# Kernel optimization log

Hardware: AMD Instinct MI355X
Metric: run time of the kernel (lower is better)

## Reference

```python
import math
import jax, jax.numpy as jnp
import numpy as np

N = 100_000          # nodes
D = 128              # sample.num_node_features
E = 1_600_000        # edges (avg degree 16)
ACM = 4              # augmented_channels_multiplier
C = 128              # channels = 4*4*channels_optuna(=8)
RATIO = 0.7          # topk_ratio + 0.1
FINAL_NODES = 3


def setup_inputs() -> dict:
    key = jax.random.key(0)
    ks = jax.random.split(key, 14)
    s = 0.05
    x = jax.random.normal(ks[0], (N, D), jnp.float32)
    edge_index = jax.random.randint(ks[1], (2, E), 0, N, dtype=jnp.int32)
    # dense_input GraphConv(D, ACM): called with empty edges -> only lin_root weight + lin_rel bias matter
    Wd_root = jax.random.normal(ks[2], (ACM, D), jnp.float32) * s
    bd = jax.random.normal(ks[3], (ACM,), jnp.float32) * s
    # input GraphConv(ACM, C)
    Wi_rel = jax.random.normal(ks[4], (C, ACM), jnp.float32) * s
    bi = jax.random.normal(ks[5], (C,), jnp.float32) * s
    Wi_root = jax.random.normal(ks[6], (C, ACM), jnp.float32) * s
    # TopKPooling(C) attention vector
    p = jax.random.normal(ks[7], (C,), jnp.float32) * s
    # conv1 GraphConv(C, 2C)
    W1_rel = jax.random.normal(ks[8], (2 * C, C), jnp.float32) * s
    b1 = jax.random.normal(ks[9], (2 * C,), jnp.float32) * s
    W1_root = jax.random.normal(ks[10], (2 * C, C), jnp.float32) * s
    # output Linear(3 * 2C, 1)
    Wo = jax.random.normal(ks[11], (1, FINAL_NODES * 2 * C), jnp.float32) * s
    bo = jax.random.normal(ks[12], (1,), jnp.float32) * s
    return {"x": x, "edge_index": edge_index, "Wd_root": Wd_root, "bd": bd,
            "Wi_rel": Wi_rel, "bi": bi, "Wi_root": Wi_root, "p": p,
            "W1_rel": W1_rel, "b1": b1, "W1_root": W1_root, "Wo": Wo, "bo": bo}


def reference(x, edge_index, Wd_root, bd, Wi_rel, bi, Wi_root, p, W1_rel, b1, W1_root, Wo, bo):
    n = x.shape[0]
    src, dst = edge_index[0], edge_index[1]  # messages flow src -> dst

    # dense_input GraphConv with empty edge set: aggr == 0 -> lin_rel bias + lin_root(x)
    h = jax.nn.gelu(x @ Wd_root.T + bd, approximate=False)               # [N, ACM]

    # input GraphConv(ACM, C): out = lin_rel(sum_j x_j) + lin_root(x)
    aggr = jax.ops.segment_sum(h[src], dst, num_segments=n)              # [N, ACM]
    h = jax.nn.gelu(aggr @ Wi_rel.T + bi + h @ Wi_root.T, approximate=False)  # [N, C]

    # TopKPooling(C, ratio=0.7): score = tanh(x.p / ||p||), keep top-k, scale kept x by score
    k = int(math.ceil(RATIO * n))
    score = jnp.tanh((h @ p) / jnp.linalg.norm(p))                        # [N]
    top_scores, perm = jax.lax.top_k(score, k)
    hp = h[perm] * top_scores[:, None]                                    # [k, C]
    # remap edges: kept node -> new index, dropped -> sentinel k
    inv = jnp.full((n,), k, dtype=jnp.int32).at[perm].set(jnp.arange(k, dtype=jnp.int32))
    ns, nd = inv[src], inv[dst]
    valid = (ns < k) & (nd < k)

    # conv1 GraphConv(C, 2C) on coarsened graph (masked scatter, sentinel row dropped)
    msg = jnp.where(valid[:, None], hp[jnp.minimum(ns, k - 1)], 0.0)      # [E, C]
    aggr = jax.ops.segment_sum(msg, jnp.where(valid, nd, k), num_segments=k + 1)[:k]
    h2 = jax.nn.gelu(aggr @ W1_rel.T + b1 + hp @ W1_root.T, approximate=False)  # [k, 2C]

    # avg_pool_x with cluster = i % 3 over single-graph batch
    cluster = jnp.arange(k, dtype=jnp.int32) % FINAL_NODES
    sums = jax.ops.segment_sum(h2, cluster, num_segments=FINAL_NODES)
    counts = jax.ops.segment_sum(jnp.ones((k,), h2.dtype), cluster, num_segments=FINAL_NODES)
    pooled = sums / counts[:, None]                                       # [3, 2C]

    # output Linear on flattened vector -> shape [1]
    return pooled.reshape(-1) @ Wo.T + bo
```

## Files before the change

### kernel.cpp

```cpp
#include <hip/hip_runtime.h>
#include <stdint.h>

#define N_NODES 100000
#define D_FEAT  128
#define E_EDGES 1600000
#define ACMC    4
#define CCH     128
#define C2CH    256
#define KKEEP   70000
#define KPAD    70016
#define NBLK    547
#define BINCAP  64
#define NBINS   (1 << 20)
#define NWIN    8
#define WWIN    12500

#define NB_BUILD (1563 * NWIN)
#define NB_H1    (N_NODES / 4)
#define NB_WCONV 128
#define NB_FRONT (NB_BUILD + NB_H1 + NB_WCONV)

typedef unsigned int u32;
typedef unsigned long long u64;
typedef unsigned short u16;
typedef short bf16x8 __attribute__((ext_vector_type(8)));
typedef float f32x4 __attribute__((ext_vector_type(4)));
typedef int i32x4 __attribute__((ext_vector_type(4)));

__device__ __forceinline__ float gelu_exact(float v){
    return 0.5f * v * (1.0f + erff(v * 0.70710678118654752440f));
}
__device__ __forceinline__ float bflo(u32 v){ return __uint_as_float(v << 16); }
__device__ __forceinline__ float bfhi(u32 v){ return __uint_as_float(v & 0xFFFF0000u); }
__device__ __forceinline__ u16 f2bf(float f){
    u32 x = __float_as_uint(f);
    return (u16)((x + 0x7FFFu + ((x >> 16) & 1u)) >> 16);
}

__global__ __launch_bounds__(256) void k_front(const int* __restrict__ ei,
                                               int* __restrict__ deg,
                                               int* __restrict__ slot,
                                               const float* __restrict__ x,
                                               const float* __restrict__ Wd,
                                               const float* __restrict__ bd,
                                               float* __restrict__ h1,
                                               const float* __restrict__ Wrel,
                                               const float* __restrict__ Wroot,
                                               u16* __restrict__ wcat) {
    int b = blockIdx.x;
    if (b < NB_BUILD) {
        int win = b & (NWIN - 1);
        int chunk = b >> 3;
        int e0 = (chunk * 256 + threadIdx.x) * 4;
        if (e0 >= E_EDGES) return;
        i32x4 dv = __builtin_nontemporal_load((const i32x4*)(ei + E_EDGES + e0));
        i32x4 sv = __builtin_nontemporal_load((const i32x4*)(ei + e0));
        int lo = win * WWIN, hi = lo + WWIN;
        #pragma unroll
        for (int j = 0; j < 4; j++) {
            int d = dv[j];
            if (d >= lo && d < hi) {
                int pos = atomicAdd(&deg[d], 1);
                if (pos < BINCAP) slot[d * BINCAP + pos] = sv[j];
            }
        }
        return;
    }
    if (b < NB_BUILD + NB_H1) {
        int tid = threadIdx.x;
        int wid = tid >> 6, lane = tid & 63;
        int node = (b - NB_BUILD) * 4 + wid;
        const float2* xr = (const float2*)(x + (size_t)node * D_FEAT);
        float2 v = xr[lane];
        const float2* wd = (const float2*)Wd;
        float s[4];
        #pragma unroll
        for (int j = 0; j < 4; j++) {
            float2 w = wd[j * 64 + lane];
            s[j] = v.x * w.x + v.y * w.y;
        }
        #pragma unroll
        for (int off = 32; off > 0; off >>= 1) {
            #pragma unroll
            for (int j = 0; j < 4; j++) s[j] += __shfl_xor(s[j], off);
        }
        if (lane == 0) {
            float4 o;
            o.x = gelu_exact(s[0] + bd[0]);
            o.y = gelu_exact(s[1] + bd[1]);
            o.z = gelu_exact(s[2] + bd[2]);
            o.w = gelu_exact(s[3] + bd[3]);
            ((float4*)h1)[node] = o;
        }
        return;
    }
    {
        int g = (b - NB_BUILD - NB_H1) * 256 + threadIdx.x;
        int ch = g >> 7, t = g & 127;
        wcat[(size_t)ch * 256 + t]       = f2bf(Wrel[(size_t)ch * 128 + t]);
        wcat[(size_t)ch * 256 + 128 + t] = f2bf(Wroot[(size_t)ch * 128 + t]);
    }
}

__global__ __launch_bounds__(256) void k_aggr1g(const int* __restrict__ deg,
                                                const int* __restrict__ slot,
                                                const float* __restrict__ h1,
                                                float* __restrict__ aggr1) {
    int d = blockIdx.x * blockDim.x + threadIdx.x;
    if (d >= N_NODES) return;
    int cnt = deg[d]; if (cnt > BINCAP) cnt = BINCAP;
    int base = d * BINCAP;
    float4 acc = make_float4(0.f, 0.f, 0.f, 0.f);
    for (int i0 = 0; i0 < cnt; i0 += 8) {
        int m = cnt - i0; if (m > 8) m = 8;
        int ss[8];
        #pragma unroll
        for (int j = 0; j < 8; j++) {
            int sj = slot[base + i0 + j];
            ss[j] = (j < m) ? sj : 0;
        }
        float4 vv[8];
        #pragma unroll
        for (int j = 0; j < 8; j++) vv[j] = ((const float4*)h1)[ss[j]];
        #pragma unroll
        for (int j = 0; j < 8; j++) {
            float msk = (j < m) ? 1.f : 0.f;
            acc.x += msk * vv[j].x;
            acc.y += msk * vv[j].y;
            acc.z += msk * vv[j].z;
            acc.w += msk * vv[j].w;
        }
    }
    ((float4*)aggr1)[d] = acc;
}

__global__ __launch_bounds__(256) void k_h_score(const float* __restrict__ aggr1,
                                                 const float* __restrict__ h1,
                                                 const float* __restrict__ Wi_rel,
                                                 const float* __restrict__ bi,
                                                 const float* __restrict__ Wi_root,
                                                 const float* __restrict__ p,
                                                 u16* __restrict__ hsb,
                                                 u32* __restrict__ dkey,
                                                 int* __restrict__ hist) {
    __shared__ float4 swr[128], swo[128];
    __shared__ float sbi[128], spv[128];
    __shared__ float spred[2];
    __shared__ float red[2][2];
    __shared__ float sscore[2];
    int tid = threadIdx.x;
    if (tid < 128) {
        swr[tid] = ((const float4*)Wi_rel)[tid];
        swo[tid] = ((const float4*)Wi_root)[tid];
        sbi[tid] = bi[tid];
        spv[tid] = p[tid];
    }
    __syncthreads();
    if (tid < 128) {
        float pp = spv[tid] * spv[tid];
        #pragma unroll
        for (int off = 32; off > 0; off >>= 1) pp += __shfl_xor(pp, off);
        if ((tid & 63) == 0) spred[tid >> 6] = pp;
    }
    __syncthreads();
    float pnorm = sqrtf(spred[0] + spred[1]);

    int half = tid >> 7;
    int c = tid & 127;
    int wih = (tid >> 6) & 1;
    int lane = tid & 63;
    float4 wr = swr[c], wo = swo[c];
    float bic = sbi[c], pc = spv[c];

    for (int node = blockIdx.x * 2 + half; node < N_NODES; node += gridDim.x * 2) {
        float4 ag = ((const float4*)aggr1)[node];
        float4 hv = ((const float4*)h1)[node];
        float val = ag.x * wr.x + ag.y * wr.y + ag.z * wr.z + ag.w * wr.w
                  + hv.x * wo.x + hv.y * wo.y + hv.z * wo.z + hv.w * wo.w
                  + bic;
        float g = gelu_exact(val);
        float hp = g * pc;
        #pragma unroll
        for (int off = 32; off > 0; off >>= 1) hp += __shfl_xor(hp, off);
        if (lane == 0) red[half][wih] = hp;
        __syncthreads();
        if (c == 0) {
            float H = red[half][0] + red[half][1];
            float sc = tanhf(H / pnorm);
            sscore[half] = sc;
            u32 u = __float_as_uint(sc);
            u32 asc = (u & 0x80000000u) ? ~u : (u | 0x80000000u);
            u32 d = ~asc;
            dkey[node] = d;
            atomicAdd(&hist[d >> 12], 1);
        }
        __syncthreads();
        hsb[(size_t)node * CCH + c] = f2bf(g * sscore[half]);
        __syncthreads();
    }
}

__global__ __launch_bounds__(1024) void k_scan1(const int* __restrict__ hist,
                                                int* __restrict__ cursor,
                                                int* __restrict__ bsum) {
    __shared__ int s[1024];
    int t = threadIdx.x;
    int g = blockIdx.x * 1024 + t;
    int v = hist[g];
    s[t] = v;
    __syncthreads();
    #pragma unroll
    for (int off = 1; off < 1024; off <<= 1) {
        int o = (t >= off) ? s[t - off] : 0;
        __syncthreads();
        s[t] += o;
        __syncthreads();
    }
    cursor[g] = s[t] - v;
    if (t == 1023) bsum[blockIdx.x] = s[t];
}

__global__ __launch_bounds__(1024) void k_scan2(int* __restrict__ bsum) {
    __shared__ int s[1024];
    int t = threadIdx.x;
    int v = bsum[t];
    s[t] = v;
    __syncthreads();
    #pragma unroll
    for (int off = 1; off < 1024; off <<= 1) {
        int o = (t >= off) ? s[t - off] : 0;
        __syncthreads();
        s[t] += o;
        __syncthreads();
    }
    bsum[t] = s[t] - v;
}

__global__ __launch_bounds__(1024) void k_scan3(int* __restrict__ cursor,
                                                const int* __restrict__ bsum) {
    int t = threadIdx.x;
    int g = blockIdx.x * 1024 + t;
    cursor[g] += bsum[blockIdx.x];
}

__global__ __launch_bounds__(256) void k_scatter(const u32* __restrict__ dkey,
                                                 int* __restrict__ cursor,
                                                 u64* __restrict__ out64) {
    int i = blockIdx.x * blockDim.x + threadIdx.x;
    if (i >= N_NODES) return;
    u32 d = dkey[i];
    int pos = atomicAdd(&cursor[d >> 12], 1);
    out64[pos] = (((u64)d) << 32) | (u32)i;
}

__global__ __launch_bounds__(256) void k_refine(const u64* __restrict__ out64,
                                                const int* __restrict__ cursor,
                                                const int* __restrict__ hist,
                                                int* __restrict__ rank,
                                                int* __restrict__ noder) {
    int pp = blockIdx.x * blockDim.x + threadIdx.x;
    if (pp >= N_NODES) return;
    u64 kp = out64[pp];
    u32 b = (u32)(kp >> 44);
    int end = cursor[b];
    int cnt = hist[b];
    int start = end - cnt;
    int r = start;
    if (cnt > 1) {
        int c = 0;
        for (int q = start; q < end; q++) c += (out64[q] < kp) ? 1 : 0;
        r = start + c;
    }
    int node = (int)(u32)kp;
    rank[node] = r;
    noder[r] = node;
}

__global__ __launch_bounds__(256) void k_gather(const int* __restrict__ deg,
                                                const int* __restrict__ slot,
                                                const int* __restrict__ rank,
                                                const u32* __restrict__ hsb32,
                                                u32* __restrict__ inb32) {
    int tid = threadIdx.x;
    int wid = tid >> 6, lane = tid & 63;
    int d = blockIdx.x * 4 + wid;
    if (d >= N_NODES) return;
    int rd = rank[d];
    if (rd >= KKEEP) return;
    int cnt = deg[d]; if (cnt > BINCAP) cnt = BINCAP;
    int base = d * BINCAP;
    float ax = 0.f, ay = 0.f;
    for (int i0 = 0; i0 < cnt; i0 += 16) {
        int m = cnt - i0; if (m > 16) m = 16;
        int ss[16];
        #pragma unroll
        for (int j = 0; j < 16; j++) {
            int sj = slot[base + i0 + j];
            ss[j] = (j < m) ? sj : 0;
        }
        int rr[16];
        u32 vv[16];
        #pragma unroll
        for (int j = 0; j < 16; j++) {
            rr[j] = rank[ss[j]];
            vv[j] = hsb32[(size_t)ss[j] * 64 + lane];
        }
        #pragma unroll
        for (int j = 0; j < 16; j++) {
            float msk = (j < m && rr[j] < KKEEP) ? 1.f : 0.f;
            ax += msk * bflo(vv[j]);
            ay += msk * bfhi(vv[j]);
        }
    }
    inb32[(size_t)rd * 128 + lane] = (u32)f2bf(ax) | ((u32)f2bf(ay) << 16);
}

__global__ __launch_bounds__(256) void k_pack(const int* __restrict__ noder,
                                              const u32* __restrict__ hsb32,
                                              u32* __restrict__ inb32) {
    int tid = threadIdx.x;
    int wave = tid >> 6, lane = tid & 63;
    int r = blockIdx.x * 4 + wave;
    if (r >= KPAD) return;
    if (r < KKEEP) {
        int n = noder[r];
        inb32[(size_t)r * 128 + 64 + lane] = hsb32[(size_t)n * 64 + lane];
    } else {
        inb32[(size_t)r * 128 + lane] = 0;
        inb32[(size_t)r * 128 + 64 + lane] = 0;
    }
}

__global__ __launch_bounds__(512, 2) void k_h2mfma(const u16* __restrict__ inb,
                                                   const u16* __restrict__ wcat,
                                                   const float* __restrict__ b1,
                                                   float* __restrict__ partial) {
    __shared__ u16 bs[256 * 256];
    __shared__ float ps[768];
    int tid = threadIdx.x;
    int blk = blockIdx.x;

    {
        int ch = tid >> 1;
        int seg = tid & 1;
        const char* src = (const char*)wcat + (size_t)ch * 512 + seg * 256;
        char* dst = (char*)bs + (size_t)ch * 512;
        int swz = (ch & 7) << 4;
        #pragma unroll
        for (int i = 0; i < 16; i++) {
            int k = seg * 256 + i * 16;
            *(i32x4*)(dst + (k ^ swz)) = *(const i32x4*)(src + i * 16);
        }
    }
    for (int i = tid; i < 768; i += 512) ps[i] = 0.f;
    __syncthreads();

    int lane = tid & 63, wave = tid >> 6;
    int wm = wave >> 1, wn = wave & 1;
    int col = lane & 15, quad = lane >> 4;
    int rbase = blk * 128 + wm * 32;
    int chbase = wn * 128;

    bf16x8 a[2][8];
    #pragma unroll
    for (int m = 0; m < 2; m++) {
        const char* ar = (const char*)inb + (size_t)(rbase + m * 16 + col) * 512 + quad * 16;
        #pragma unroll
        for (int k0 = 0; k0 < 8; k0++)
            a[m][k0] = *(const bf16x8*)(ar + k0 * 64);
    }

    f32x4 acc[2][8];
    #pragma unroll
    for (int m = 0; m < 2; m++)
        #pragma unroll
        for (int n = 0; n < 8; n++)
            acc[m][n] = (f32x4){0.f, 0.f, 0.f, 0.f};

    int swzr = (col & 7) << 4;
    #pragma unroll
    for (int k0 = 0; k0 < 8; k0++) {
        int kb = k0 * 64 + quad * 16;
        bf16x8 b[8];
        #pragma unroll
        for (int n = 0; n < 8; n++) {
            int ch = chbase + n * 16 + col;
            b[n] = *(const bf16x8*)((const char*)bs + (size_t)ch * 512 + (kb ^ swzr));
        }
        #pragma unroll
        for (int n = 0; n < 8; n++) {
            acc[0][n] = __builtin_amdgcn_mfma_f32_16x16x32_bf16(a[0][k0], b[n], acc[0][n], 0, 0, 0);
            acc[1][n] = __builtin_amdgcn_mfma_f32_16x16x32_bf16(a[1][k0], b[n], acc[1][n], 0, 0, 0);
        }
    }

    #pragma unroll
    for (int m = 0; m < 2; m++) {
        #pragma unroll
        for (int n = 0; n < 8; n++) {
            int ch = chbase + n * 16 + col;
            float bias = b1[ch];
            float p0 = 0.f, p1 = 0.f, p2 = 0.f;
            #pragma unroll
            for (int reg = 0; reg < 4; reg++) {
                int r = rbase + m * 16 + quad * 4 + reg;
                float g = (r < KKEEP) ? gelu_exact(acc[m][n][reg] + bias) : 0.f;
                int md = r % 3;
                if (md == 0) p0 += g; else if (md == 1) p1 += g; else p2 += g;
            }
            p0 += __shfl_xor(p0, 16); p0 += __shfl_xor(p0, 32);
            p1 += __shfl_xor(p1, 16); p1 += __shfl_xor(p1, 32);
            p2 += __shfl_xor(p2, 16); p2 += __shfl_xor(p2, 32);
            if (quad == 0) {
                atomicAdd(&ps[0 * 256 + ch], p0);
                atomicAdd(&ps[1 * 256 + ch], p1);
                atomicAdd(&ps[2 * 256 + ch], p2);
            }
        }
    }
    __syncthreads();
    for (int i = tid; i < 768; i += 512)
        partial[(size_t)blk * 768 + i] = ps[i];
}

__global__ __launch_bounds__(64) void k_poolred(const float* __restrict__ partial,
                                                float* __restrict__ pooled) {
    int j = blockIdx.x;
    int lane = threadIdx.x;
    float s = 0.f;
    for (int i = lane; i < NBLK; i += 64)
        s += partial[(size_t)i * 768 + j];
    #pragma unroll
    for (int off = 32; off > 0; off >>= 1) s += __shfl_xor(s, off);
    if (lane == 0) pooled[j] = s;
}

__global__ __launch_bounds__(768) void k_out(const float* __restrict__ pooled,
                                             const float* __restrict__ Wo,
                                             const float* __restrict__ bo,
                                             float* __restrict__ out) {
    __shared__ float red[12];
    int t = threadIdx.x;
    int ci = t >> 8;
    float cnt = (ci == 0) ? 23334.0f : 23333.0f;
    float acc = (pooled[t] / cnt) * Wo[t];
    #pragma unroll
    for (int off = 32; off > 0; off >>= 1) acc += __shfl_xor(acc, off);
    int wid = t >> 6, lane = t & 63;
    if (lane == 0) red[wid] = acc;
    __syncthreads();
    if (t == 0) {
        float s = 0.0f;
        #pragma unroll
        for (int w = 0; w < 12; w++) s += red[w];
        out[0] = s + bo[0];
    }
}

extern "C" void kernel_launch(void* const* d_in, const int* in_sizes, int n_in,
                              void* d_out, int out_size, void* d_ws, size_t ws_size,
                              hipStream_t stream) {
    const float* x       = (const float*)d_in[0];
    const int*   ei      = (const int*)d_in[1];
    const float* Wd      = (const float*)d_in[2];
    const float* bd      = (const float*)d_in[3];
    const float* Wi_rel  = (const float*)d_in[4];
    const float* bi      = (const float*)d_in[5];
    const float* Wi_root = (const float*)d_in[6];
    const float* p       = (const float*)d_in[7];
    const float* W1_rel  = (const float*)d_in[8];
    const float* b1      = (const float*)d_in[9];
    const float* W1_root = (const float*)d_in[10];
    const float* Wo      = (const float*)d_in[11];
    const float* bo      = (const float*)d_in[12];

    char* ws = (char*)d_ws;
    size_t off_b = 0;
    auto alloc = [&](size_t bytes) -> void* {
        void* ptr = ws + off_b;
        off_b += (bytes + 255) & ~(size_t)255;
        return ptr;
    };
    float* h1     = (float*)alloc((size_t)N_NODES * 4 * sizeof(float));
    float* aggr1  = (float*)alloc((size_t)N_NODES * 4 * sizeof(float));
    u16*   hsb    = (u16*)alloc((size_t)N_NODES * CCH * sizeof(u16));
    u32*   dkey   = (u32*)alloc((size_t)N_NODES * sizeof(u32));
    int*   rank   = (int*)alloc((size_t)N_NODES * sizeof(int));
    int*   noder  = (int*)alloc((size_t)N_NODES * sizeof(int));
    int*   deg    = (int*)alloc((size_t)N_NODES * sizeof(int));
    int*   slot   = (int*)alloc((size_t)N_NODES * BINCAP * sizeof(int));
    u16*   inb    = (u16*)alloc((size_t)KPAD * C2CH * sizeof(u16));
    u16*   wcat   = (u16*)alloc((size_t)C2CH * 256 * sizeof(u16));
    float* partial= (float*)alloc((size_t)NBLK * 768 * sizeof(float));
    float* pooled = (float*)alloc(768 * sizeof(float));
    (void)ws_size; (void)in_sizes; (void)n_in; (void)out_size;

    int* hist   = (int*)inb;
    int* cursor = (int*)inb + NBINS;
    u64* out64  = (u64*)((int*)inb + 2 * NBINS);
    int* bsum   = (int*)(out64 + N_NODES);

    hipMemsetAsync(deg, 0, (size_t)N_NODES * sizeof(int), stream);
    hipMemsetAsync(hist, 0, (size_t)NBINS * sizeof(int), stream);

    k_front<<<NB_FRONT, 256, 0, stream>>>(ei, deg, slot, x, Wd, bd, h1,
                                          W1_rel, W1_root, wcat);

    k_aggr1g<<<(N_NODES + 255) / 256, 256, 0, stream>>>(deg, slot, h1, aggr1);
    k_h_score<<<2048, 256, 0, stream>>>(aggr1, h1, Wi_rel, bi, Wi_root, p,
                                        hsb, dkey, hist);

    k_scan1<<<NBINS / 1024, 1024, 0, stream>>>(hist, cursor, bsum);
    k_scan2<<<1, 1024, 0, stream>>>(bsum);
    k_scan3<<<NBINS / 1024, 1024, 0, stream>>>(cursor, bsum);
    k_scatter<<<(N_NODES + 255) / 256, 256, 0, stream>>>(dkey, cursor, out64);
    k_refine<<<(N_NODES + 255) / 256, 256, 0, stream>>>(out64, cursor, hist, rank, noder);

    k_gather<<<(N_NODES + 3) / 4, 256, 0, stream>>>(deg, slot, rank,
                                                    (const u32*)hsb, (u32*)inb);
    k_pack<<<(KPAD + 3) / 4, 256, 0, stream>>>(noder, (const u32*)hsb, (u32*)inb);
    k_h2mfma<<<NBLK, 512, 0, stream>>>(inb, wcat, b1, partial);
    k_poolred<<<768, 64, 0, stream>>>(partial, pooled);
    k_out<<<1, 768, 0, stream>>>(pooled, Wo, bo, (float*)d_out);
}
```

Measured before the change: 415.9 us.

## Replace fixed-capacity adjacency bins with exact CSR built via degree count and scan

Builds the destination adjacency as a compact CSR: a degree-count pass, an exclusive scan into row pointers, then a windowed scatter of source ids. This replaces the 64-slot-per-node bins, which took 25.6 MB of sparse storage and silently truncated high-degree nodes. The cost is an extra pass over the edge list and three extra small kernels. The histogram scan also moves to a wave-shuffle scan with 16 elements per thread, and the pooled reduction is reorganised into 12 blocks that read coalesced rows.

```diff
diff --git a/kernel.cpp b/kernel.cpp
--- a/kernel.cpp
+++ b/kernel.cpp
@@ -10,15 +10,14 @@
 #define KKEEP   70000
 #define KPAD    70016
 #define NBLK    547
-#define BINCAP  64
 #define NBINS   (1 << 20)
 #define NWIN    8
 #define WWIN    12500
 
-#define NB_BUILD (1563 * NWIN)
+#define NB_HIST  1563
 #define NB_H1    (N_NODES / 4)
 #define NB_WCONV 128
-#define NB_FRONT (NB_BUILD + NB_H1 + NB_WCONV)
+#define NB_FRONT (NB_HIST + NB_H1 + NB_WCONV)
 
 typedef unsigned int u32;
 typedef unsigned long long u64;
@@ -39,7 +38,6 @@
 
 __global__ __launch_bounds__(256) void k_front(const int* __restrict__ ei,
                                                int* __restrict__ deg,
-                                               int* __restrict__ slot,
                                                const float* __restrict__ x,
                                                const float* __restrict__ Wd,
                                                const float* __restrict__ bd,
@@ -48,28 +46,18 @@
                                                const float* __restrict__ Wroot,
                                                u16* __restrict__ wcat) {
     int b = blockIdx.x;
-    if (b < NB_BUILD) {
-        int win = b & (NWIN - 1);
-        int chunk = b >> 3;
-        int e0 = (chunk * 256 + threadIdx.x) * 4;
+    if (b < NB_HIST) {
+        int e0 = (b * 256 + threadIdx.x) * 4;
         if (e0 >= E_EDGES) return;
         i32x4 dv = __builtin_nontemporal_load((const i32x4*)(ei + E_EDGES + e0));
-        i32x4 sv = __builtin_nontemporal_load((const i32x4*)(ei + e0));
-        int lo = win * WWIN, hi = lo + WWIN;
-        #pragma unroll
-        for (int j = 0; j < 4; j++) {
-            int d = dv[j];
-            if (d >= lo && d < hi) {
-                int pos = atomicAdd(&deg[d], 1);
-                if (pos < BINCAP) slot[d * BINCAP + pos] = sv[j];
-            }
-        }
+        #pragma unroll
+        for (int j = 0; j < 4; j++) atomicAdd(&deg[dv[j]], 1);
         return;
     }
-    if (b < NB_BUILD + NB_H1) {
+    if (b < NB_HIST + NB_H1) {
         int tid = threadIdx.x;
         int wid = tid >> 6, lane = tid & 63;
-        int node = (b - NB_BUILD) * 4 + wid;
+        int node = (b - NB_HIST) * 4 + wid;
         const float2* xr = (const float2*)(x + (size_t)node * D_FEAT);
         float2 v = xr[lane];
         const float2* wd = (const float2*)Wd;
@@ -95,29 +83,127 @@
         return;
     }
     {
-        int g = (b - NB_BUILD - NB_H1) * 256 + threadIdx.x;
+        int g = (b - NB_HIST - NB_H1) * 256 + threadIdx.x;
         int ch = g >> 7, t = g & 127;
         wcat[(size_t)ch * 256 + t]       = f2bf(Wrel[(size_t)ch * 128 + t]);
         wcat[(size_t)ch * 256 + 128 + t] = f2bf(Wroot[(size_t)ch * 128 + t]);
     }
 }
 
+__global__ __launch_bounds__(256) void k_escan1(const int* __restrict__ in,
+                                                int* __restrict__ out,
+                                                int* __restrict__ bsum,
+                                                int n) {
+    __shared__ int wsum[4];
+    int tid = threadIdx.x;
+    int lane = tid & 63, wave = tid >> 6;
+    int base = blockIdx.x * 4096 + tid * 16;
+    int o[16];
+    #pragma unroll
+    for (int i = 0; i < 16; i++) {
+        int g = base + i;
+        o[i] = (g < n) ? in[g] : 0;
+    }
+    int ex[16];
+    int run = 0;
+    #pragma unroll
+    for (int i = 0; i < 16; i++) { ex[i] = run; run += o[i]; }
+    int inc = run;
+    #pragma unroll
+    for (int off = 1; off < 64; off <<= 1) {
+        int t = __shfl_up(inc, off);
+        if (lane >= off) inc += t;
+    }
+    int wexc = inc - run;
+    if (lane == 63) wsum[wave] = inc;
+    __syncthreads();
+    int wbase = 0;
+    #pragma unroll
+    for (int w = 0; w < 4; w++) wbase += (w < wave) ? wsum[w] : 0;
+    int tbase = wbase + wexc;
+    #pragma unroll
+    for (int i = 0; i < 16; i++) {
+        int g = base + i;
+        if (g < n) out[g] = tbase + ex[i];
+    }
+    if (tid == 255) bsum[blockIdx.x] = wbase + inc;
+}
+
+__global__ __launch_bounds__(256) void k_escan2(int* __restrict__ bsum, int n) {
+    __shared__ int wsum[4];
+    int tid = threadIdx.x;
+    int lane = tid & 63, wave = tid >> 6;
+    int val = (tid < n) ? bsum[tid] : 0;
+    int inc = val;
+    #pragma unroll
+    for (int off = 1; off < 64; off <<= 1) {
+        int t = __shfl_up(inc, off);
+        if (lane >= off) inc += t;
+    }
+    int wexc = inc - val;
+    if (lane == 63) wsum[wave] = inc;
+    __syncthreads();
+    int wbase = 0;
+    #pragma unroll
+    for (int w = 0; w < 4; w++) wbase += (w < wave) ? wsum[w] : 0;
+    if (tid < n) bsum[tid] = wbase + wexc;
+}
+
+__global__ __launch_bounds__(256) void k_escan3(int* __restrict__ out,
+                                                const int* __restrict__ bsum,
+                                                int* __restrict__ dup,
+                                                int n) {
+    int add = bsum[blockIdx.x];
+    int base = blockIdx.x * 4096 + threadIdx.x * 16;
+    #pragma unroll
+    for (int i = 0; i < 16; i++) {
+        int g = base + i;
+        if (g < n) {
+            int t = out[g] + add;
+            out[g] = t;
+            if (dup) dup[g] = t;
+        }
+    }
+}
+
+__global__ __launch_bounds__(256) void k_scatter_e(const int* __restrict__ ei,
+                                                   int* __restrict__ ecur,
+                                                   int* __restrict__ adj) {
+    int b = blockIdx.x;
+    int win = b & (NWIN - 1);
+    int chunk = b >> 3;
+    int e0 = (chunk * 256 + threadIdx.x) * 4;
+    if (e0 >= E_EDGES) return;
+    i32x4 dv = __builtin_nontemporal_load((const i32x4*)(ei + E_EDGES + e0));
+    i32x4 sv = __builtin_nontemporal_load((const i32x4*)(ei + e0));
+    int lo = win * WWIN, hi = lo + WWIN;
+    #pragma unroll
+    for (int j = 0; j < 4; j++) {
+        int d = dv[j];
+        if (d >= lo && d < hi) {
+            int pos = atomicAdd(&ecur[d], 1);
+            adj[pos] = sv[j];
+        }
+    }
+}
+
 __global__ __launch_bounds__(256) void k_aggr1g(const int* __restrict__ deg,
-                                                const int* __restrict__ slot,
+                                                const int* __restrict__ rowptr,
+                                                const int* __restrict__ adj,
                                                 const float* __restrict__ h1,
                                                 float* __restrict__ aggr1) {
     int d = blockIdx.x * blockDim.x + threadIdx.x;
     if (d >= N_NODES) return;
-    int cnt = deg[d]; if (cnt > BINCAP) cnt = BINCAP;
-    int base = d * BINCAP;
+    int cnt = deg[d];
+    int base = rowptr[d];
     float4 acc = make_float4(0.f, 0.f, 0.f, 0.f);
     for (int i0 = 0; i0 < cnt; i0 += 8) {
         int m = cnt - i0; if (m > 8) m = 8;
         int ss[8];
         #pragma unroll
         for (int j = 0; j < 8; j++) {
-            int sj = slot[base + i0 + j];
-            ss[j] = (j < m) ? sj : 0;
+            int sj = adj[base + i0 + ((j < m) ? j : 0)];
+            ss[j] = sj;
         }
         float4 vv[8];
         #pragma unroll
@@ -200,49 +286,6 @@
     }
 }
 
-__global__ __launch_bounds__(1024) void k_scan1(const int* __restrict__ hist,
-                                                int* __restrict__ cursor,
-                                                int* __restrict__ bsum) {
-    __shared__ int s[1024];
-    int t = threadIdx.x;
-    int g = blockIdx.x * 1024 + t;
-    int v = hist[g];
-    s[t] = v;
-    __syncthreads();
-    #pragma unroll
-    for (int off = 1; off < 1024; off <<= 1) {
-        int o = (t >= off) ? s[t - off] : 0;
-        __syncthreads();
-        s[t] += o;
-        __syncthreads();
-    }
-    cursor[g] = s[t] - v;
-    if (t == 1023) bsum[blockIdx.x] = s[t];
-}
-
-__global__ __launch_bounds__(1024) void k_scan2(int* __restrict__ bsum) {
-    __shared__ int s[1024];
-    int t = threadIdx.x;
-    int v = bsum[t];
-    s[t] = v;
-    __syncthreads();
-    #pragma unroll
-    for (int off = 1; off < 1024; off <<= 1) {
-        int o = (t >= off) ? s[t - off] : 0;
-        __syncthreads();
-        s[t] += o;
-        __syncthreads();
-    }
-    bsum[t] = s[t] - v;
-}
-
-__global__ __launch_bounds__(1024) void k_scan3(int* __restrict__ cursor,
-                                                const int* __restrict__ bsum) {
-    int t = threadIdx.x;
-    int g = blockIdx.x * 1024 + t;
-    cursor[g] += bsum[blockIdx.x];
-}
-
 __global__ __launch_bounds__(256) void k_scatter(const u32* __restrict__ dkey,
                                                  int* __restrict__ cursor,
                                                  u64* __restrict__ out64) {
@@ -277,7 +320,8 @@
 }
 
 __global__ __launch_bounds__(256) void k_gather(const int* __restrict__ deg,
-                                                const int* __restrict__ slot,
+                                                const int* __restrict__ rowptr,
+                                                const int* __restrict__ adj,
                                                 const int* __restrict__ rank,
                                                 const u32* __restrict__ hsb32,
                                                 u32* __restrict__ inb32) {
@@ -287,17 +331,15 @@
     if (d >= N_NODES) return;
     int rd = rank[d];
     if (rd >= KKEEP) return;
-    int cnt = deg[d]; if (cnt > BINCAP) cnt = BINCAP;
-    int base = d * BINCAP;
+    int cnt = deg[d];
+    int base = rowptr[d];
     float ax = 0.f, ay = 0.f;
     for (int i0 = 0; i0 < cnt; i0 += 16) {
         int m = cnt - i0; if (m > 16) m = 16;
         int ss[16];
         #pragma unroll
-        for (int j = 0; j < 16; j++) {
-            int sj = slot[base + i0 + j];
-            ss[j] = (j < m) ? sj : 0;
-        }
+        for (int j = 0; j < 16; j++)
+            ss[j] = adj[base + i0 + ((j < m) ? j : 0)];
         int rr[16];
         u32 vv[16];
         #pragma unroll
@@ -423,16 +465,18 @@
         partial[(size_t)blk * 768 + i] = ps[i];
 }
 
-__global__ __launch_bounds__(64) void k_poolred(const float* __restrict__ partial,
-                                                float* __restrict__ pooled) {
-    int j = blockIdx.x;
-    int lane = threadIdx.x;
+__global__ __launch_bounds__(256) void k_poolred(const float* __restrict__ partial,
+                                                 float* __restrict__ pooled) {
+    __shared__ float red[4][64];
+    int tid = threadIdx.x, lane = tid & 63, wave = tid >> 6;
+    int j = blockIdx.x * 64 + lane;
     float s = 0.f;
-    for (int i = lane; i < NBLK; i += 64)
+    for (int i = wave; i < NBLK; i += 4)
         s += partial[(size_t)i * 768 + j];
-    #pragma unroll
-    for (int off = 32; off > 0; off >>= 1) s += __shfl_xor(s, off);
-    if (lane == 0) pooled[j] = s;
+    red[wave][lane] = s;
+    __syncthreads();
+    if (wave == 0)
+        pooled[j] = (red[0][lane] + red[1][lane]) + (red[2][lane] + red[3][lane]);
 }
 
 __global__ __launch_bounds__(768) void k_out(const float* __restrict__ pooled,
@@ -488,7 +532,10 @@
     int*   rank   = (int*)alloc((size_t)N_NODES * sizeof(int));
     int*   noder  = (int*)alloc((size_t)N_NODES * sizeof(int));
     int*   deg    = (int*)alloc((size_t)N_NODES * sizeof(int));
-    int*   slot   = (int*)alloc((size_t)N_NODES * BINCAP * sizeof(int));
+    int*   rowptr = (int*)alloc((size_t)102400 * sizeof(int));
+    int*   ecur   = (int*)alloc((size_t)102400 * sizeof(int));
+    int*   adj    = (int*)alloc((size_t)E_EDGES * sizeof(int));
+    int*   bsumA  = (int*)alloc(256 * sizeof(int));
     u16*   inb    = (u16*)alloc((size_t)KPAD * C2CH * sizeof(u16));
     u16*   wcat   = (u16*)alloc((size_t)C2CH * 256 * sizeof(u16));
     float* partial= (float*)alloc((size_t)NBLK * 768 * sizeof(float));
@@ -503,23 +550,29 @@
     hipMemsetAsync(deg, 0, (size_t)N_NODES * sizeof(int), stream);
     hipMemsetAsync(hist, 0, (size_t)NBINS * sizeof(int), stream);
 
-    k_front<<<NB_FRONT, 256, 0, stream>>>(ei, deg, slot, x, Wd, bd, h1,
+    k_front<<<NB_FRONT, 256, 0, stream>>>(ei, deg, x, Wd, bd, h1,
                                           W1_rel, W1_root, wcat);
 
-    k_aggr1g<<<(N_NODES + 255) / 256, 256, 0, stream>>>(deg, slot, h1, aggr1);
+    k_escan1<<<25, 256, 0, stream>>>(deg, rowptr, bsumA, N_NODES);
+    k_escan2<<<1, 256, 0, stream>>>(bsumA, 25);
+    k_escan3<<<25, 256, 0, stream>>>(rowptr, bsumA, ecur, N_NODES);
+
+    k_scatter_e<<<1563 * NWIN, 256, 0, stream>>>(ei, ecur, adj);
+
+    k_aggr1g<<<(N_NODES + 255) / 256, 256, 0, stream>>>(deg, rowptr, adj, h1, aggr1);
     k_h_score<<<2048, 256, 0, stream>>>(aggr1, h1, Wi_rel, bi, Wi_root, p,
                                         hsb, dkey, hist);
 
-    k_scan1<<<NBINS / 1024, 1024, 0, stream>>>(hist, cursor, bsum);
-    k_scan2<<<1, 1024, 0, stream>>>(bsum);
-    k_scan3<<<NBINS / 1024, 1024, 0, stream>>>(cursor, bsum);
+    k_escan1<<<NBINS / 4096, 256, 0, stream>>>(hist, cursor, bsum, NBINS);
+    k_escan2<<<1, 256, 0, stream>>>(bsum, 256);
+    k_escan3<<<NBINS / 4096, 256, 0, stream>>>(cursor, bsum, (int*)nullptr, NBINS);
     k_scatter<<<(N_NODES + 255) / 256, 256, 0, stream>>>(dkey, cursor, out64);
     k_refine<<<(N_NODES + 255) / 256, 256, 0, stream>>>(out64, cursor, hist, rank, noder);
 
-    k_gather<<<(N_NODES + 3) / 4, 256, 0, stream>>>(deg, slot, rank,
+    k_gather<<<(N_NODES + 3) / 4, 256, 0, stream>>>(deg, rowptr, adj, rank,
                                                     (const u32*)hsb, (u32*)inb);
     k_pack<<<(KPAD + 3) / 4, 256, 0, stream>>>(noder, (const u32*)hsb, (u32*)inb);
     k_h2mfma<<<NBLK, 512, 0, stream>>>(inb, wcat, b1, partial);
-    k_poolred<<<768, 64, 0, stream>>>(partial, pooled);
+    k_poolred<<<12, 256, 0, stream>>>(partial, pooled);
     k_out<<<1, 768, 0, stream>>>(pooled, Wo, bo, (float*)d_out);
 }
```

Result: slower. 535.3 us (+28.7%).
